# Kernel tuning notes

Hardware: AMD Instinct MI355X
Metric: run time of the kernel (lower is better)

Reference implementation:

```python
import jax, jax.numpy as jnp
import numpy as np

D_MODEL = 1024
N_HEAD = 16
HEAD_DIM = D_MODEL // N_HEAD
BATCH = 2
SEQ = 2048


def setup_inputs() -> dict:
    key = jax.random.key(0)
    ks = jax.random.split(key, 5)
    std = np.sqrt(2.0 / (D_MODEL + D_MODEL)).astype(np.float32)
    return {
        "in_features": jax.random.normal(ks[0], (BATCH, SEQ, D_MODEL), dtype=jnp.float32),
        "Wq": jax.random.normal(ks[1], (D_MODEL, D_MODEL), dtype=jnp.float32) * std,
        "Wk": jax.random.normal(ks[2], (D_MODEL, D_MODEL), dtype=jnp.float32) * std,
        "Wv": jax.random.normal(ks[3], (D_MODEL, D_MODEL), dtype=jnp.float32) * std,
        "Wo": jax.random.normal(ks[4], (D_MODEL, D_MODEL), dtype=jnp.float32) * std,
    }


def reference(in_features, Wq, Wk, Wv, Wo):
    B, S, _ = in_features.shape
    # projections: x @ W (custom Linear stores weight as [in, out], no bias)
    q = (in_features @ Wq).reshape(B, S, N_HEAD, HEAD_DIM).transpose(0, 2, 1, 3)  # [B,H,S,Dh]
    k = (in_features @ Wk).reshape(B, S, N_HEAD, HEAD_DIM).transpose(0, 2, 1, 3)
    v = (in_features @ Wv).reshape(B, S, N_HEAD, HEAD_DIM).transpose(0, 2, 1, 3)
    scale = HEAD_DIM ** (-0.5)
    scores = jnp.einsum("bhqd,bhkd->bhqk", q, k) * scale  # [B,H,S,S]
    causal = jnp.tril(jnp.ones((S, S), dtype=bool))
    scores = jnp.where(causal, scores, -jnp.inf)
    attn = jax.nn.softmax(scores, axis=-1)
    ctx = jnp.einsum("bhqk,bhkd->bhqd", attn, v)  # [B,H,S,Dh]
    ctx = ctx.transpose(0, 2, 1, 3).reshape(B, S, D_MODEL)
    return ctx @ Wo
```

## Files before the change

### kernel.cpp

```cpp
#include <hip/hip_runtime.h>
#include <hip/hip_bf16.h>

#define DM 1024
#define NH 16
#define HD 64
#define B_ 2
#define S_ 2048
#define M_ (B_*S_)

typedef __attribute__((ext_vector_type(8))) short bf16x8;
typedef __attribute__((ext_vector_type(4))) float f32x4;

__device__ __forceinline__ float bf2f(ushort u) {
  union { unsigned u32; float f; } c; c.u32 = ((unsigned)u) << 16; return c.f;
}
__device__ __forceinline__ ushort f2bf(float f) {
  union { float f; unsigned u32; } c; c.f = f;
  unsigned u = c.u32;
  unsigned r = (u + 0x7fffu + ((u >> 16) & 1u)) >> 16;
  return (ushort)r;
}
__device__ __forceinline__ unsigned fbits(float f) {
  union { float f; unsigned u; } c; c.f = f; return c.u;
}

__device__ __forceinline__ void async16(const ushort* g, ushort* l) {
  __builtin_amdgcn_global_load_lds((const __attribute__((address_space(1))) void*)g,
                                   (__attribute__((address_space(3))) void*)l, 16, 0, 0);
}

__global__ void cvt_x(const float* __restrict__ x, ushort* __restrict__ xb) {
  int i = blockIdx.x * blockDim.x + threadIdx.x;
  float4 v = ((const float4*)x)[i];
  ushort4 o;
  o.x = f2bf(v.x); o.y = f2bf(v.y); o.z = f2bf(v.z); o.w = f2bf(v.w);
  ((ushort4*)xb)[i] = o;
}

__global__ void cvt_transpose_w(const float* __restrict__ W0, const float* __restrict__ W1,
                                const float* __restrict__ W2, const float* __restrict__ W3,
                                ushort* __restrict__ wt) {
  __shared__ float tile[64][65];
  int z = blockIdx.z;
  const float* W = (z == 0) ? W0 : (z == 1) ? W1 : (z == 2) ? W2 : W3;
  ushort* Wt = wt + (size_t)z * (DM * DM);
  int tx = threadIdx.x, ty = threadIdx.y;
  int c0 = blockIdx.x * 64, r0 = blockIdx.y * 64;
  #pragma unroll
  for (int i = ty; i < 64; i += 4) tile[i][tx] = W[(size_t)(r0 + i) * DM + c0 + tx];
  __syncthreads();
  #pragma unroll
  for (int i = ty; i < 64; i += 4) Wt[(size_t)(c0 + i) * DM + r0 + tx] = f2bf(tile[tx][i]);
}

template <int MODE>
__device__ __forceinline__ void gemm_body(const ushort* __restrict__ A,
                                          const ushort* __restrict__ Bt,
                                          ushort* __restrict__ Cb,
                                          float* __restrict__ Cf) {
  __shared__ __align__(16) ushort As[128 * 32];
  __shared__ __align__(16) ushort Bs[128 * 32];
  const int K = DM;
  int m0 = blockIdx.y * 128;
  int n0 = blockIdx.x * 128;
  int t = threadIdx.x;
  int lane = t & 63, wave = t >> 6;
  int wm = (wave >> 1) * 64, wn = (wave & 1) * 64;
  int lrow = lane & 15, quad = lane >> 4;

  int Ra = wave * 32;
  int srow = lane >> 2, scol = (lane & 3) * 8;

  f32x4 acc[4][4];
  #pragma unroll
  for (int r = 0; r < 4; ++r)
    #pragma unroll
    for (int c = 0; c < 4; ++c) acc[r][c] = (f32x4){0.f, 0.f, 0.f, 0.f};

  for (int k0 = 0; k0 < K; k0 += 32) {
    const ushort* ga = A + (size_t)(m0 + Ra + srow) * K + k0 + scol;
    const ushort* gb = Bt + (size_t)(n0 + Ra + srow) * K + k0 + scol;
    async16(ga,            As + Ra * 32);
    async16(ga + 16 * K,   As + (Ra + 16) * 32);
    async16(gb,            Bs + Ra * 32);
    async16(gb + 16 * K,   Bs + (Ra + 16) * 32);
    __syncthreads();

    bf16x8 af[4], bfr[4];
    #pragma unroll
    for (int r = 0; r < 4; ++r)
      af[r] = *(const bf16x8*)(As + (wm + r * 16 + lrow) * 32 + quad * 8);
    #pragma unroll
    for (int c = 0; c < 4; ++c)
      bfr[c] = *(const bf16x8*)(Bs + (wn + c * 16 + lrow) * 32 + quad * 8);
    #pragma unroll
    for (int r = 0; r < 4; ++r)
      #pragma unroll
      for (int c = 0; c < 4; ++c)
        acc[r][c] = __builtin_amdgcn_mfma_f32_16x16x32_bf16(af[r], bfr[c], acc[r][c], 0, 0, 0);
    __syncthreads();
  }

  #pragma unroll
  for (int r = 0; r < 4; ++r) {
    #pragma unroll
    for (int c = 0; c < 4; ++c) {
      #pragma unroll
      for (int e = 0; e < 4; ++e) {
        int m = m0 + wm + r * 16 + quad * 4 + e;
        int n = n0 + wn + c * 16 + lrow;
        if (MODE == 0) {
          Cf[(size_t)m * DM + n] = acc[r][c][e];
        } else if (MODE == 1) {
          int b = m >> 11, s = m & 2047, h = n >> 6, d = n & 63;
          Cb[(((size_t)(b * NH + h)) * S_ + s) * HD + d] = f2bf(acc[r][c][e]);
        } else {
          int b = m >> 11, s = m & 2047, h = n >> 6, d = n & 63;
          Cb[(((size_t)(b * NH + h)) * HD + d) * S_ + s] = f2bf(acc[r][c][e]);
        }
      }
    }
  }
}

__global__ __launch_bounds__(256, 2) void gemm_qkv(const ushort* __restrict__ A,
                                                   const ushort* __restrict__ wt,
                                                   ushort* __restrict__ qkv) {
  int z = blockIdx.z;
  if (z < 2)
    gemm_body<1>(A, wt + (size_t)z * (DM * DM), qkv + (size_t)z * ((size_t)M_ * DM), nullptr);
  else
    gemm_body<2>(A, wt + (size_t)z * (DM * DM), qkv + (size_t)z * ((size_t)M_ * DM), nullptr);
}

__global__ __launch_bounds__(256, 2) void gemm_out(const ushort* __restrict__ A,
                                                   const ushort* __restrict__ wt,
                                                   float* __restrict__ C) {
  gemm_body<0>(A, wt, nullptr, C);
}

struct AttnState {
  f32x4 o[4];
  float l;
};

__device__ __forceinline__ void attn_tile_compute(
    int q0, int kt, bf16x8 qf0, bf16x8 qf1,
    const bf16x8 kf0[4], const bf16x8 kf1[4],
    const bf16x8 vf0[4], const bf16x8 vf1[4],
    ushort* pl, AttnState& st, int lrow, int quad) {
  f32x4 s[4];
  #pragma unroll
  for (int c = 0; c < 4; ++c) {
    f32x4 z = (f32x4){0.f, 0.f, 0.f, 0.f};
    z = __builtin_amdgcn_mfma_f32_16x16x32_bf16(kf0[c], qf0, z, 0, 0, 0);
    z = __builtin_amdgcn_mfma_f32_16x16x32_bf16(kf1[c], qf1, z, 0, 0, 0);
    s[c] = z;
  }
  int q = q0 + lrow;
  #pragma unroll
  for (int c = 0; c < 4; ++c) {
    float pv[4];
    #pragma unroll
    for (int e = 0; e < 4; ++e) {
      int key = kt + c * 16 + quad * 4 + e;
      float v = __expf(s[c][e] * 0.125f);
      v = (key <= q) ? v : 0.f;
      pv[e] = v;
      st.l += v;
    }
    uint2 pk;
    pk.x = __builtin_amdgcn_perm(fbits(pv[1]), fbits(pv[0]), 0x07060302u);
    pk.y = __builtin_amdgcn_perm(fbits(pv[3]), fbits(pv[2]), 0x07060302u);
    *(uint2*)(pl + lrow * 72 + c * 16 + quad * 4) = pk;
  }
  bf16x8 pf0 = *(const bf16x8*)(pl + lrow * 72 + quad * 8);
  bf16x8 pf1 = *(const bf16x8*)(pl + lrow * 72 + 32 + quad * 8);
  #pragma unroll
  for (int dt = 0; dt < 4; ++dt) {
    st.o[dt] = __builtin_amdgcn_mfma_f32_16x16x32_bf16(pf0, vf0[dt], st.o[dt], 0, 0, 0);
    st.o[dt] = __builtin_amdgcn_mfma_f32_16x16x32_bf16(pf1, vf1[dt], st.o[dt], 0, 0, 0);
  }
}

__global__ __launch_bounds__(256, 2) void attn_mfma(const ushort* __restrict__ Q,
                                                    const ushort* __restrict__ Kmat,
                                                    const ushort* __restrict__ Vt,
                                                    ushort* __restrict__ ctx) {
  __shared__ __align__(16) ushort Ks[2][64 * 72];
  __shared__ __align__(16) ushort Vs[2][64 * 72];
  __shared__ __align__(16) ushort plds[4][16 * 72];
  int t = threadIdx.x;
  int lane = t & 63, wave = t >> 6;
  int lrow = lane & 15, quad = lane >> 4;
  int bh = blockIdx.y;
  int p = blockIdx.x;
  int qt_lo = p, qt_hi = 31 - p;
  const ushort* Kb = Kmat + (size_t)bh * S_ * HD;
  const ushort* Vb = Vt + (size_t)bh * HD * S_;
  ushort* pl = plds[wave];
  int b = bh >> 4, h = bh & 15;

  int r0 = t >> 3, s0 = (t & 7) * 8;
  int r1 = (t + 256) >> 3, s1 = s0;

  int q0_lo = qt_lo * 64 + wave * 16;
  int q0_hi = qt_hi * 64 + wave * 16;
  const ushort* Qlo = Q + ((size_t)bh * S_ + q0_lo) * HD;
  const ushort* Qhi = Q + ((size_t)bh * S_ + q0_hi) * HD;
  bf16x8 qlo0 = *(const bf16x8*)(Qlo + (size_t)lrow * HD + quad * 8);
  bf16x8 qlo1 = *(const bf16x8*)(Qlo + (size_t)lrow * HD + 32 + quad * 8);
  bf16x8 qhi0 = *(const bf16x8*)(Qhi + (size_t)lrow * HD + quad * 8);
  bf16x8 qhi1 = *(const bf16x8*)(Qhi + (size_t)lrow * HD + 32 + quad * 8);

  AttnState lo, hi;
  #pragma unroll
  for (int i = 0; i < 4; ++i) {
    lo.o[i] = (f32x4){0.f, 0.f, 0.f, 0.f}; hi.o[i] = (f32x4){0.f, 0.f, 0.f, 0.f};
  }
  lo.l = 0.f; hi.l = 0.f;

  int kend = qt_hi * 64;

  {
    uint4 ka = *(const uint4*)(Kb + (size_t)r0 * HD + s0);
    uint4 kb2 = *(const uint4*)(Kb + (size_t)r1 * HD + s1);
    uint4 va = *(const uint4*)(Vb + (size_t)r0 * S_ + s0);
    uint4 vb2 = *(const uint4*)(Vb + (size_t)r1 * S_ + s1);
    *(uint4*)(Ks[0] + r0 * 72 + s0) = ka;
    *(uint4*)(Ks[0] + r1 * 72 + s1) = kb2;
    *(uint4*)(Vs[0] + r0 * 72 + s0) = va;
    *(uint4*)(Vs[0] + r1 * 72 + s1) = vb2;
  }
  __syncthreads();

  for (int kt = 0; kt <= kend; kt += 64) {
    int cur = (kt >> 6) & 1, nxt = cur ^ 1;
    bool has_next = (kt < kend);

    uint4 ka, kb2, va, vb2;
    if (has_next) {
      int ktn = kt + 64;
      ka  = *(const uint4*)(Kb + (size_t)(ktn + r0) * HD + s0);
      kb2 = *(const uint4*)(Kb + (size_t)(ktn + r1) * HD + s1);
      va  = *(const uint4*)(Vb + (size_t)r0 * S_ + ktn + s0);
      vb2 = *(const uint4*)(Vb + (size_t)r1 * S_ + ktn + s1);
    }

    bf16x8 kf0[4], kf1[4], vf0[4], vf1[4];
    #pragma unroll
    for (int c = 0; c < 4; ++c) {
      const ushort* kr = Ks[cur] + (c * 16 + lrow) * 72;
      kf0[c] = *(const bf16x8*)(kr + quad * 8);
      kf1[c] = *(const bf16x8*)(kr + 32 + quad * 8);
      const ushort* vr = Vs[cur] + (c * 16 + lrow) * 72;
      vf0[c] = *(const bf16x8*)(vr + quad * 8);
      vf1[c] = *(const bf16x8*)(vr + 32 + quad * 8);
    }

    attn_tile_compute(q0_hi, kt, qhi0, qhi1, kf0, kf1, vf0, vf1, pl, hi, lrow, quad);
    if (kt <= qt_lo * 64)
      attn_tile_compute(q0_lo, kt, qlo0, qlo1, kf0, kf1, vf0, vf1, pl, lo, lrow, quad);

    if (has_next) {
      *(uint4*)(Ks[nxt] + r0 * 72 + s0) = ka;
      *(uint4*)(Ks[nxt] + r1 * 72 + s1) = kb2;
      *(uint4*)(Vs[nxt] + r0 * 72 + s0) = va;
      *(uint4*)(Vs[nxt] + r1 * 72 + s1) = vb2;
    }
    __syncthreads();
  }

  #pragma unroll
  for (int half = 0; half < 2; ++half) {
    AttnState& st = half ? hi : lo;
    int q0 = half ? q0_hi : q0_lo;
    float l = st.l;
    l += __shfl_xor(l, 16);
    l += __shfl_xor(l, 32);
    float rl = 1.0f / l;
    #pragma unroll
    for (int e = 0; e < 4; ++e) {
      float rinv = __shfl(rl, quad * 4 + e);
      int q = q0 + quad * 4 + e;
      #pragma unroll
      for (int dt = 0; dt < 4; ++dt)
        ctx[((size_t)b * S_ + q) * DM + h * HD + dt * 16 + lrow] = f2bf(st.o[dt][e] * rinv);
    }
  }
}

extern "C" void kernel_launch(void* const* d_in, const int* in_sizes, int n_in,
                              void* d_out, int out_size, void* d_ws, size_t ws_size,
                              hipStream_t stream) {
  const float* x  = (const float*)d_in[0];
  const float* Wq = (const float*)d_in[1];
  const float* Wk = (const float*)d_in[2];
  const float* Wv = (const float*)d_in[3];
  const float* Wo = (const float*)d_in[4];
  float* out = (float*)d_out;
  ushort* ws = (ushort*)d_ws;

  ushort* xb  = ws;
  ushort* wt  = xb + (size_t)M_ * DM;
  ushort* qkv = wt + (size_t)4 * DM * DM;
  ushort* ctx = qkv + (size_t)3 * M_ * DM;

  cvt_x<<<dim3((M_ * DM) / 4 / 256), 256, 0, stream>>>(x, xb);
  cvt_transpose_w<<<dim3(16, 16, 4), dim3(64, 4), 0, stream>>>(Wq, Wk, Wv, Wo, wt);
  gemm_qkv<<<dim3(DM / 128, M_ / 128, 3), 256, 0, stream>>>(xb, wt, qkv);
  attn_mfma<<<dim3(16, B_ * NH), 256, 0, stream>>>(qkv, qkv + (size_t)M_ * DM,
                                                   qkv + (size_t)2 * M_ * DM, ctx);
  gemm_out<<<dim3(DM / 128, M_ / 128), 256, 0, stream>>>(ctx, wt + (size_t)3 * DM * DM, out);
}
```

Baseline: 189.7 us.

## Stage V-transpose epilogue through LDS and skip causal masking on interior tiles

The V projection epilogue used to write scattered 2-byte transposed stores. It now stages each 64-row half of the accumulator tile through shared memory, so the [B,H,D,S] layout can be written with coalesced 16-byte stores. The V GEMM is split into its own kernel with extra LDS, which costs one more launch and may lower occupancy. The attention kernel also templates the tile compute on masking, so only diagonal tiles evaluate the causal mask, and exp is computed via exp2 with a folded scale constant.

```diff
diff --git a/kernel.cpp b/kernel.cpp
--- a/kernel.cpp
+++ b/kernel.cpp
@@ -57,9 +57,8 @@
 __device__ __forceinline__ void gemm_body(const ushort* __restrict__ A,
                                           const ushort* __restrict__ Bt,
                                           ushort* __restrict__ Cb,
-                                          float* __restrict__ Cf) {
-  __shared__ __align__(16) ushort As[128 * 32];
-  __shared__ __align__(16) ushort Bs[128 * 32];
+                                          float* __restrict__ Cf,
+                                          ushort* As, ushort* Bs, ushort* Ts) {
   const int K = DM;
   int m0 = blockIdx.y * 128;
   int n0 = blockIdx.x * 128;
@@ -101,49 +100,91 @@
     __syncthreads();
   }
 
-  #pragma unroll
-  for (int r = 0; r < 4; ++r) {
-    #pragma unroll
-    for (int c = 0; c < 4; ++c) {
+  if constexpr (MODE == 2) {
+    int bb = m0 >> 11;
+    int s0base = m0 & 2047;
+    #pragma unroll
+    for (int H = 0; H < 2; ++H) {
+      __syncthreads();
+      if ((wave >> 1) == H) {
+        #pragma unroll
+        for (int r = 0; r < 4; ++r)
+          #pragma unroll
+          for (int c = 0; c < 4; ++c) {
+            uint2 pk;
+            pk.x = (unsigned)f2bf(acc[r][c][0]) | ((unsigned)f2bf(acc[r][c][1]) << 16);
+            pk.y = (unsigned)f2bf(acc[r][c][2]) | ((unsigned)f2bf(acc[r][c][3]) << 16);
+            *(uint2*)(Ts + (wn + c * 16 + lrow) * 72 + r * 16 + quad * 4) = pk;
+          }
+      }
+      __syncthreads();
       #pragma unroll
-      for (int e = 0; e < 4; ++e) {
-        int m = m0 + wm + r * 16 + quad * 4 + e;
-        int n = n0 + wn + c * 16 + lrow;
-        if (MODE == 0) {
-          Cf[(size_t)m * DM + n] = acc[r][c][e];
-        } else if (MODE == 1) {
-          int b = m >> 11, s = m & 2047, h = n >> 6, d = n & 63;
-          Cb[(((size_t)(b * NH + h)) * S_ + s) * HD + d] = f2bf(acc[r][c][e]);
-        } else {
-          int b = m >> 11, s = m & 2047, h = n >> 6, d = n & 63;
-          Cb[(((size_t)(b * NH + h)) * HD + d) * S_ + s] = f2bf(acc[r][c][e]);
+      for (int i = 0; i < 4; ++i) {
+        int id = t + i * 256;
+        int nn = id >> 3, col = (id & 7) * 8;
+        uint4 v = *(const uint4*)(Ts + nn * 72 + col);
+        int h2 = (n0 >> 6) + (nn >> 6), d2 = nn & 63;
+        size_t dst = (((size_t)(bb * NH + h2)) * HD + d2) * (size_t)S_ + s0base + H * 64 + col;
+        *(uint4*)(Cb + dst) = v;
+      }
+    }
+  } else {
+    #pragma unroll
+    for (int r = 0; r < 4; ++r) {
+      #pragma unroll
+      for (int c = 0; c < 4; ++c) {
+        #pragma unroll
+        for (int e = 0; e < 4; ++e) {
+          int m = m0 + wm + r * 16 + quad * 4 + e;
+          int n = n0 + wn + c * 16 + lrow;
+          if (MODE == 0) {
+            Cf[(size_t)m * DM + n] = acc[r][c][e];
+          } else {
+            int b = m >> 11, s = m & 2047, h = n >> 6, d = n & 63;
+            Cb[(((size_t)(b * NH + h)) * S_ + s) * HD + d] = f2bf(acc[r][c][e]);
+          }
         }
       }
     }
   }
 }
 
-__global__ __launch_bounds__(256, 2) void gemm_qkv(const ushort* __restrict__ A,
-                                                   const ushort* __restrict__ wt,
-                                                   ushort* __restrict__ qkv) {
+__global__ __launch_bounds__(256, 2) void gemm_qk(const ushort* __restrict__ A,
+                                                  const ushort* __restrict__ wt,
+                                                  ushort* __restrict__ qkv) {
+  __shared__ __align__(16) ushort As[128 * 32];
+  __shared__ __align__(16) ushort Bs[128 * 32];
   int z = blockIdx.z;
-  if (z < 2)
-    gemm_body<1>(A, wt + (size_t)z * (DM * DM), qkv + (size_t)z * ((size_t)M_ * DM), nullptr);
-  else
-    gemm_body<2>(A, wt + (size_t)z * (DM * DM), qkv + (size_t)z * ((size_t)M_ * DM), nullptr);
+  gemm_body<1>(A, wt + (size_t)z * (DM * DM), qkv + (size_t)z * ((size_t)M_ * DM),
+               nullptr, As, Bs, nullptr);
+}
+
+__global__ __launch_bounds__(256, 2) void gemm_v(const ushort* __restrict__ A,
+                                                 const ushort* __restrict__ wt,
+                                                 ushort* __restrict__ qkv) {
+  __shared__ __align__(16) ushort As[128 * 32];
+  __shared__ __align__(16) ushort Bs[128 * 32];
+  __shared__ __align__(16) ushort Ts[128 * 72];
+  gemm_body<2>(A, wt + (size_t)2 * (DM * DM), qkv + (size_t)2 * ((size_t)M_ * DM),
+               nullptr, As, Bs, Ts);
 }
 
 __global__ __launch_bounds__(256, 2) void gemm_out(const ushort* __restrict__ A,
                                                    const ushort* __restrict__ wt,
                                                    float* __restrict__ C) {
-  gemm_body<0>(A, wt, nullptr, C);
-}
+  __shared__ __align__(16) ushort As[128 * 32];
+  __shared__ __align__(16) ushort Bs[128 * 32];
+  gemm_body<0>(A, wt, nullptr, C, As, Bs, nullptr);
+}
+
+#define EXPC 0.18033688011f
 
 struct AttnState {
   f32x4 o[4];
   float l;
 };
 
+template <bool MASKED>
 __device__ __forceinline__ void attn_tile_compute(
     int q0, int kt, bf16x8 qf0, bf16x8 qf1,
     const bf16x8 kf0[4], const bf16x8 kf1[4],
@@ -163,9 +204,11 @@
     float pv[4];
     #pragma unroll
     for (int e = 0; e < 4; ++e) {
-      int key = kt + c * 16 + quad * 4 + e;
-      float v = __expf(s[c][e] * 0.125f);
-      v = (key <= q) ? v : 0.f;
+      float v = __builtin_amdgcn_exp2f(s[c][e] * EXPC);
+      if (MASKED) {
+        int key = kt + c * 16 + quad * 4 + e;
+        v = (key <= q) ? v : 0.f;
+      }
       pv[e] = v;
       st.l += v;
     }
@@ -221,6 +264,7 @@
   lo.l = 0.f; hi.l = 0.f;
 
   int kend = qt_hi * 64;
+  int lo_end = qt_lo * 64;
 
   {
     uint4 ka = *(const uint4*)(Kb + (size_t)r0 * HD + s0);
@@ -258,9 +302,14 @@
       vf1[c] = *(const bf16x8*)(vr + 32 + quad * 8);
     }
 
-    attn_tile_compute(q0_hi, kt, qhi0, qhi1, kf0, kf1, vf0, vf1, pl, hi, lrow, quad);
-    if (kt <= qt_lo * 64)
-      attn_tile_compute(q0_lo, kt, qlo0, qlo1, kf0, kf1, vf0, vf1, pl, lo, lrow, quad);
+    if (kt < kend)
+      attn_tile_compute<false>(q0_hi, kt, qhi0, qhi1, kf0, kf1, vf0, vf1, pl, hi, lrow, quad);
+    else
+      attn_tile_compute<true>(q0_hi, kt, qhi0, qhi1, kf0, kf1, vf0, vf1, pl, hi, lrow, quad);
+    if (kt < lo_end)
+      attn_tile_compute<false>(q0_lo, kt, qlo0, qlo1, kf0, kf1, vf0, vf1, pl, lo, lrow, quad);
+    else if (kt == lo_end)
+      attn_tile_compute<true>(q0_lo, kt, qlo0, qlo1, kf0, kf1, vf0, vf1, pl, lo, lrow, quad);
 
     if (has_next) {
       *(uint4*)(Ks[nxt] + r0 * 72 + s0) = ka;
@@ -308,7 +357,8 @@
 
   cvt_x<<<dim3((M_ * DM) / 4 / 256), 256, 0, stream>>>(x, xb);
   cvt_transpose_w<<<dim3(16, 16, 4), dim3(64, 4), 0, stream>>>(Wq, Wk, Wv, Wo, wt);
-  gemm_qkv<<<dim3(DM / 128, M_ / 128, 3), 256, 0, stream>>>(xb, wt, qkv);
+  gemm_qk<<<dim3(DM / 128, M_ / 128, 2), 256, 0, stream>>>(xb, wt, qkv);
+  gemm_v<<<dim3(DM / 128, M_ / 128), 256, 0, stream>>>(xb, wt, qkv);
   attn_mfma<<<dim3(16, B_ * NH), 256, 0, stream>>>(qkv, qkv + (size_t)M_ * DM,
                                                    qkv + (size_t)2 * M_ * DM, ctx);
   gemm_out<<<dim3(DM / 128, M_ / 128), 256, 0, stream>>>(ctx, wt + (size_t)3 * DM * DM, out);
```

New measurement: 213.6 us. +12.6%, slower.
